# Performance work log

Hardware: AMD Instinct MI355X
Metric: run time of the kernel (lower is better)

Reference implementation:

```python
import jax, jax.numpy as jnp
import numpy as np

C = 256; CM = 8; MAXI = 100; NCLS = 80
KP = (CM + 2) * CM + CM + CM * CM + CM + CM + 1  # 169 dynamic-kernel params

def _ln(x, g, b, eps=1e-5):
    m = x.mean(-1, keepdims=True)
    v = ((x - m) ** 2).mean(-1, keepdims=True)
    return g * (x - m) * jax.lax.rsqrt(v + eps) + b

def _mlp(x, hw, hb, lng, lnb, fw, fb):
    # torchvision MLP: [Linear -> LayerNorm -> SiLU] * n_hidden -> Linear
    for i in range(hw.shape[0]):
        x = jax.nn.silu(_ln(x @ hw[i] + hb[i], lng[i], lnb[i]))
    return x @ fw + fb

def _conv1x1_bn(x, w, s, b):
    # 1x1 conv (no bias) + inference-mode BatchNorm folded into per-channel affine
    y = jnp.einsum('bchw,oc->bohw', x, w)
    return y * s[None, :, None, None] + b[None, :, None, None]

def _grid(h, w):
    # normalized cell-center coordinates, (x, y) order, shape [h, w, 2]
    ys = (jnp.arange(h, dtype=jnp.float32) + 0.5) / h
    xs = (jnp.arange(w, dtype=jnp.float32) + 0.5) / w
    return jnp.stack([jnp.broadcast_to(xs[None, :], (h, w)),
                      jnp.broadcast_to(ys[:, None], (h, w))], axis=-1)

def setup_inputs() -> dict:
    key = jax.random.key(0)
    ks = iter(jax.random.split(key, 40))
    nrm = lambda shape, s=0.02: s * jax.random.normal(next(ks), shape, jnp.float32)
    B = 4
    inp = {
        'x0': jax.random.normal(next(ks), (B, 3, 512, 512), jnp.float32),
        'x1': jax.random.normal(next(ks), (B, 64, 256, 256), jnp.float32),
        'x2': jax.random.normal(next(ks), (B, 128, 128, 128), jnp.float32),
        'x3': jax.random.normal(next(ks), (B, 256, 64, 64), jnp.float32),
        'x4': jax.random.normal(next(ks), (B, 512, 32, 32), jnp.float32),
        'x5': jax.random.normal(next(ks), (B, 1024, 16, 16), jnp.float32),
        'lat3_w': nrm((C, 256)), 'lat3_s': jnp.ones((C,)), 'lat3_b': jnp.zeros((C,)),
        'lat4_w': nrm((C, 512)), 'lat4_s': jnp.ones((C,)), 'lat4_b': jnp.zeros((C,)),
        'lat5_w': nrm((C, 1024)), 'lat5_s': jnp.ones((C,)), 'lat5_b': jnp.zeros((C,)),
        'mlat_w': nrm((C, 256)), 'mlat_s': jnp.ones((C,)), 'mlat_b': jnp.zeros((C,)),
        'mhead_w': nrm((CM, C, 3, 3)), 'mhead_s': jnp.ones((CM,)), 'mhead_b': jnp.zeros((CM,)),
        'loc_hw': nrm((4, C, C)), 'loc_hb': jnp.zeros((4, C)), 'loc_lng': jnp.ones((4, C)), 'loc_lnb': jnp.zeros((4, C)),
        'loc_fw': nrm((C, 1)), 'loc_fb': -5.0 * jnp.ones((1,)),
        'cls_hw': nrm((4, C, C)), 'cls_hb': jnp.zeros((4, C)), 'cls_lng': jnp.ones((4, C)), 'cls_lnb': jnp.zeros((4, C)),
        'cls_fw': nrm((C, NCLS)), 'cls_fb': jnp.zeros((NCLS,)),
        'ker_hw': nrm((4, C, C)), 'ker_hb': jnp.zeros((4, C)), 'ker_lng': jnp.ones((4, C)), 'ker_lnb': jnp.zeros((4, C)),
        'ker_fw': nrm((C, KP)), 'ker_fb': jnp.zeros((KP,)),
    }
    return inp

def reference(x0, x1, x2, x3, x4, x5,
              lat3_w, lat3_s, lat3_b, lat4_w, lat4_s, lat4_b, lat5_w, lat5_s, lat5_b,
              mlat_w, mlat_s, mlat_b, mhead_w, mhead_s, mhead_b,
              loc_hw, loc_hb, loc_lng, loc_lnb, loc_fw, loc_fb,
              cls_hw, cls_hb, cls_lng, cls_lnb, cls_fw, cls_fb,
              ker_hw, ker_hb, ker_lng, ker_lnb, ker_fw, ker_fb):
    B, _, H, W = x0.shape
    lvls = [(x3, lat3_w, lat3_s, lat3_b), (x4, lat4_w, lat4_s, lat4_b), (x5, lat5_w, lat5_s, lat5_b)]
    feats = [_conv1x1_bn(x, w, s, b) for (x, w, s, b) in lvls]
    flat = jnp.concatenate([f.reshape(B, C, -1).transpose(0, 2, 1) for f in feats], axis=1)  # [B, L, C]
    loc_logits = _mlp(flat, loc_hw, loc_hb, loc_lng, loc_lnb, loc_fw, loc_fb)[..., 0]       # [B, L]
    top_vals, top_idx = jax.lax.top_k(loc_logits, MAXI)
    scores = jax.nn.sigmoid(top_vals)
    num_instances = (scores > 0.5).sum(axis=1)
    gfeat = jnp.take_along_axis(flat, top_idx[:, :, None], axis=1)  # [B, I, C]
    # mask branch
    mf = _conv1x1_bn(x3, mlat_w, mlat_s, mlat_b)
    mf = jax.lax.conv_general_dilated(mf, mhead_w, (1, 1), 'SAME', dimension_numbers=('NCHW', 'OIHW', 'NCHW'))
    mf = jax.nn.silu(mf * mhead_s[None, :, None, None] + mhead_b[None, :, None, None])  # [B, CM, h3, w3]
    h3, w3 = x3.shape[2], x3.shape[3]
    offs_flat = jnp.concatenate([_grid(x.shape[2], x.shape[3]).reshape(-1, 2) for x in (x3, x4, x5)], axis=0)
    offs = offs_flat[top_idx]                                # [B, I, 2]
    grid = _grid(h3, w3).transpose(2, 0, 1)                  # [2, h3, w3]
    grid = grid[None, None] - offs[:, :, :, None, None]      # [B, I, 2, h, w]
    mfi = jnp.broadcast_to(mf[:, None], (B, MAXI, CM, h3, w3))
    feats_i = jnp.concatenate([mfi, grid], axis=2)           # [B, I, CM+2, h, w]
    dyn = _mlp(gfeat, ker_hw, ker_hb, ker_lng, ker_lnb, ker_fw, ker_fb)  # [B, I, KP]
    c = CM
    o = (c + 2) * c
    w1 = dyn[..., :o].reshape(B, MAXI, c + 2, c)
    b1 = dyn[..., o:o + c].reshape(B, MAXI, c, 1, 1); o += c
    w2 = dyn[..., o:o + c * c].reshape(B, MAXI, c, c); o += c * c
    b2 = dyn[..., o:o + c].reshape(B, MAXI, c, 1, 1); o += c
    w3 = dyn[..., o:o + c].reshape(B, MAXI, c, 1); o += c
    b3 = dyn[..., o:].reshape(B, MAXI, 1, 1, 1)
    m = jax.nn.silu(jnp.einsum('bichw,bicd->bidhw', feats_i, w1) + b1)
    m = jax.nn.silu(jnp.einsum('bichw,bicd->bidhw', m, w2) + b2)
    m = jnp.einsum('bichw,bicd->bidhw', m, w3) + b3
    masks = jax.nn.sigmoid(m[:, :, 0])                       # [B, I, h3, w3]
    classes = jnp.argmax(_mlp(gfeat, cls_hw, cls_hb, cls_lng, cls_lnb, cls_fw, cls_fb), axis=-1)
    masks = jax.image.resize(masks, (B, MAXI, H, W), method='bilinear', antialias=False)
    return (num_instances, scores, classes, masks)
```

## Files before the change

### kernel.cpp

```cpp
#include <hip/hip_runtime.h>
#include <hip/hip_bf16.h>
#include <math.h>

#define DEVI __device__ __forceinline__

constexpr int LTOT  = 5376;
constexpr int NINST = 100;
constexpr int NCLS  = 80;
constexpr int KPAR  = 169;

DEVI float waveAllSum(float v) {
#pragma unroll
  for (int s = 32; s > 0; s >>= 1) v += __shfl_xor(v, s, 64);
  return v;
}
DEVI float siluf(float x) { return x / (1.0f + expf(-x)); }
DEVI float sigmf(float x) { return 1.0f / (1.0f + expf(-x)); }
DEVI float rdlane(float v, int lane) {
  return __int_as_float(__builtin_amdgcn_readlane(__float_as_int(v), lane));
}

__global__ __launch_bounds__(256) void wtrans(
    const float* __restrict__ w3, const float* __restrict__ w4,
    const float* __restrict__ w5, const float* __restrict__ wm,
    float* __restrict__ wt3, float* __restrict__ wt4,
    float* __restrict__ wt5, float* __restrict__ wtm)
{
  __shared__ float t[64][65];
  const int bid = blockIdx.x;
  const float* src; float* dst; int K, rel;
  if (bid < 16)       { src = w3; dst = wt3; K = 256;  rel = bid; }
  else if (bid < 48)  { src = w4; dst = wt4; K = 512;  rel = bid - 16; }
  else if (bid < 112) { src = w5; dst = wt5; K = 1024; rel = bid - 48; }
  else                { src = wm; dst = wtm; K = 256;  rel = bid - 112; }
  const int ctiles = K >> 6;
  const int ot = rel / ctiles, ct = rel % ctiles;
  const int o0 = ot * 64, c0 = ct * 64;
  const int tid = threadIdx.x;
#pragma unroll
  for (int s = 0; s < 16; ++s) {
    const int e = tid + 256*s;
    const int r = e >> 6, c = e & 63;
    t[r][c] = src[(long)(o0 + r)*K + c0 + c];
  }
  __syncthreads();
#pragma unroll
  for (int s = 0; s < 16; ++s) {
    const int e = tid + 256*s;
    const int q = e >> 6, p = e & 63;
    dst[(long)(c0 + q)*256 + o0 + p] = t[p][q];
  }
}

__global__ __launch_bounds__(256) void lateral_main(
    const float* __restrict__ x3, const float* __restrict__ x4, const float* __restrict__ x5,
    const float* __restrict__ wt3, const float* __restrict__ s3, const float* __restrict__ b3,
    const float* __restrict__ wt4, const float* __restrict__ s4, const float* __restrict__ b4,
    const float* __restrict__ wt5, const float* __restrict__ s5, const float* __restrict__ b5,
    const float* __restrict__ wtm, const float* __restrict__ sm, const float* __restrict__ bm,
    float* __restrict__ flat, float* __restrict__ mlatb)
{
  __shared__ float xs[32][36];
  __shared__ float ws[32][256];
  const int tid = threadIdx.x;
  const int rg = tid >> 6, cg = tid & 63;
  const int bid = blockIdx.x;
  const float *x, *wt, *sc, *bi;
  int K, P, b, p0, baseL = 0; bool tomlat = false;
  if (bid < 512)       { x=x3; wt=wt3; sc=s3; bi=b3; K=256;  P=4096; b=bid>>7;  p0=(bid&127)*32; }
  else if (bid < 1024) { const int rel=bid-512;  x=x3; wt=wtm; sc=sm; bi=bm; K=256;  P=4096; b=rel>>7; p0=(rel&127)*32; tomlat=true; }
  else if (bid < 1152) { const int rel=bid-1024; x=x4; wt=wt4; sc=s4; bi=b4; K=512;  P=1024; b=rel>>5; p0=(rel&31)*32; baseL=4096; }
  else                 { const int rel=bid-1152; x=x5; wt=wt5; sc=s5; bi=b5; K=1024; P=256;  b=rel>>3; p0=(rel&7)*32;  baseL=5120; }
  const float* xb = x + (long)b * K * P;
  float acc[8][4] = {};
  const int nkb = K >> 5;
  for (int kb = 0; kb < nkb; ++kb) {
    __syncthreads();
#pragma unroll
    for (int s = 0; s < 4; ++s) {
      const int e = tid + 256*s;
      const int kk = e >> 5, px = e & 31;
      xs[kk][px] = xb[(long)(kb*32 + kk)*P + p0 + px];
    }
    {
      const float4* w4p = reinterpret_cast<const float4*>(wt + (kb << 13));
#pragma unroll
      for (int q = 0; q < 8; ++q) {
        const int c = tid + (q << 8);
        *reinterpret_cast<float4*>(&ws[c >> 6][4*(c & 63)]) = w4p[c];
      }
    }
    __syncthreads();
#pragma unroll
    for (int kk = 0; kk < 32; ++kk) {
      const float4 a0 = *reinterpret_cast<const float4*>(&xs[kk][8*rg]);
      const float4 a1 = *reinterpret_cast<const float4*>(&xs[kk][8*rg+4]);
      const float ar[8] = {a0.x,a0.y,a0.z,a0.w,a1.x,a1.y,a1.z,a1.w};
      const float4 wv = *reinterpret_cast<const float4*>(&ws[kk][4*cg]);
#pragma unroll
      for (int i = 0; i < 8; ++i) {
        acc[i][0] += ar[i]*wv.x; acc[i][1] += ar[i]*wv.y;
        acc[i][2] += ar[i]*wv.z; acc[i][3] += ar[i]*wv.w;
      }
    }
  }
  const float4 sA = *reinterpret_cast<const float4*>(&sc[4*cg]);
  const float4 bA = *reinterpret_cast<const float4*>(&bi[4*cg]);
  if (!tomlat) {
#pragma unroll
    for (int i = 0; i < 8; ++i) {
      const float4 ov = { acc[i][0]*sA.x+bA.x, acc[i][1]*sA.y+bA.y,
                          acc[i][2]*sA.z+bA.z, acc[i][3]*sA.w+bA.w };
      *reinterpret_cast<float4*>(&flat[((long)b*LTOT + baseL + p0 + 8*rg + i)*256 + 4*cg]) = ov;
    }
  } else {
#pragma unroll
    for (int j = 0; j < 4; ++j) {
      const float sj = (&sA.x)[j], bj = (&bA.x)[j];
      const float4 o0 = { acc[0][j]*sj+bj, acc[1][j]*sj+bj, acc[2][j]*sj+bj, acc[3][j]*sj+bj };
      const float4 o1 = { acc[4][j]*sj+bj, acc[5][j]*sj+bj, acc[6][j]*sj+bj, acc[7][j]*sj+bj };
      float* mb = &mlatb[((long)b*256 + 4*cg + j)*4096 + p0 + 8*rg];
      *reinterpret_cast<float4*>(mb) = o0;
      *reinterpret_cast<float4*>(mb + 4) = o1;
    }
  }
}

__global__ __launch_bounds__(256, 4) void loc4(
    const float* __restrict__ in, const float* __restrict__ hw,
    const float* __restrict__ hb, const float* __restrict__ lng, const float* __restrict__ lnb,
    const float* __restrict__ fw, const float* __restrict__ fb, float* __restrict__ logits)
{
  const int tid = threadIdx.x;
  const int rg = tid >> 6, cg = tid & 63;
  const long r0 = (long)blockIdx.x * 32 + rg * 8;
  float xv[8][4];
#pragma unroll
  for (int i = 0; i < 8; ++i) {
    const float4 v = *reinterpret_cast<const float4*>(&in[(r0 + i)*256 + 4*cg]);
    xv[i][0]=v.x; xv[i][1]=v.y; xv[i][2]=v.z; xv[i][3]=v.w;
  }
  for (int L = 0; L < 4; ++L) {
    const float* w = hw + L*65536 + 4*cg;
    float acc[8][4] = {};
    for (int kb = 0; kb < 256; kb += 8) {
      float4 wv[8];
#pragma unroll
      for (int u = 0; u < 8; ++u)
        wv[u] = *reinterpret_cast<const float4*>(&w[(kb + u) << 8]);
#pragma unroll
      for (int u = 0; u < 8; ++u) {
        const int lanek = (kb >> 2) + (u >> 2);
#pragma unroll
        for (int i = 0; i < 8; ++i) {
          const float a = rdlane(xv[i][u & 3], lanek);
          acc[i][0] += a*wv[u].x; acc[i][1] += a*wv[u].y;
          acc[i][2] += a*wv[u].z; acc[i][3] += a*wv[u].w;
        }
      }
    }
    const float4 hb4 = *reinterpret_cast<const float4*>(&hb[L*256 + 4*cg]);
    const float4 g4  = *reinterpret_cast<const float4*>(&lng[L*256 + 4*cg]);
    const float4 lb4 = *reinterpret_cast<const float4*>(&lnb[L*256 + 4*cg]);
#pragma unroll
    for (int i = 0; i < 8; ++i) {
      const float y0 = acc[i][0]+hb4.x, y1 = acc[i][1]+hb4.y;
      const float y2 = acc[i][2]+hb4.z, y3 = acc[i][3]+hb4.w;
      const float m = waveAllSum(y0+y1+y2+y3) * (1.0f/256.0f);
      const float d0=y0-m, d1=y1-m, d2=y2-m, d3=y3-m;
      const float var = waveAllSum(d0*d0+d1*d1+d2*d2+d3*d3) * (1.0f/256.0f);
      const float rs = rsqrtf(var + 1e-5f);
      xv[i][0] = siluf(g4.x*d0*rs + lb4.x);
      xv[i][1] = siluf(g4.y*d1*rs + lb4.y);
      xv[i][2] = siluf(g4.z*d2*rs + lb4.z);
      xv[i][3] = siluf(g4.w*d3*rs + lb4.w);
    }
  }
  const float4 fw4 = *reinterpret_cast<const float4*>(&fw[4*cg]);
  const float fbv = fb[0];
#pragma unroll
  for (int i = 0; i < 8; ++i) {
    float d = xv[i][0]*fw4.x + xv[i][1]*fw4.y + xv[i][2]*fw4.z + xv[i][3]*fw4.w;
    d = waveAllSum(d);
    if (cg == 0) logits[r0 + i] = d + fbv;
  }
}

__global__ __launch_bounds__(256) void topk_gather(
    const float* __restrict__ logits, const float* __restrict__ flat,
    int* __restrict__ topi, float* __restrict__ gfeat,
    float* __restrict__ dout)
{
  __shared__ float sv[LTOT];
  __shared__ float rv[4];
  __shared__ int   ri[4];
  __shared__ int   sidx[NINST];
  const int b = blockIdx.x, tid = threadIdx.x;
  for (int l = tid; l < LTOT; l += 256) sv[l] = logits[b*LTOT + l];
  __syncthreads();
  int cnt = 0;
  for (int t = 0; t < NINST; ++t) {
    float bv = -INFINITY; int bidx = 0x7fffffff;
    for (int l = tid; l < LTOT; l += 256) {
      const float v = sv[l];
      if (v > bv) { bv = v; bidx = l; }
    }
#pragma unroll
    for (int s = 32; s > 0; s >>= 1) {
      const float v2 = __shfl_xor(bv, s, 64);
      const int   i2 = __shfl_xor(bidx, s, 64);
      if (v2 > bv || (v2 == bv && i2 < bidx)) { bv = v2; bidx = i2; }
    }
    if ((tid & 63) == 0) { rv[tid >> 6] = bv; ri[tid >> 6] = bidx; }
    __syncthreads();
    if (tid == 0) {
      bv = rv[0]; bidx = ri[0];
#pragma unroll
      for (int q = 1; q < 4; ++q)
        if (rv[q] > bv || (rv[q] == bv && ri[q] < bidx)) { bv = rv[q]; bidx = ri[q]; }
      sidx[t] = bidx; topi[b*NINST + t] = bidx;
      dout[4 + b*NINST + t] = sigmf(bv);
      if (bv > 0.0f) ++cnt;
      sv[bidx] = -INFINITY;
    }
    __syncthreads();
  }
  if (tid == 0) dout[b] = (float)cnt;
  for (int t = 0; t < NINST; ++t) {
    const int ix = sidx[t];
    gfeat[((long)b*NINST + t)*256 + tid] = flat[((long)b*LTOT + ix)*256 + tid];
  }
}

__global__ __launch_bounds__(256) void clsker4(
    const float* __restrict__ gfeat, float* __restrict__ h2,
    const float* __restrict__ chw, const float* __restrict__ chb,
    const float* __restrict__ cg_, const float* __restrict__ cb_,
    const float* __restrict__ khw, const float* __restrict__ khb,
    const float* __restrict__ kg_, const float* __restrict__ kb_)
{
  __shared__ float xs[256][12];
  __shared__ float wsm[16][256];
  const int tid = threadIdx.x;
  const int rg = tid >> 6, cg = tid & 63;
  const bool ker = blockIdx.x >= 50;
  const int r0 = (ker ? (blockIdx.x - 50) : blockIdx.x) * 8;
  const int outr0 = r0 + (ker ? 400 : 0);
  const float* hw = ker ? khw : chw;
  const float* hb = ker ? khb : chb;
  const float* g_ = ker ? kg_ : cg_;
  const float* lb = ker ? kb_ : cb_;
#pragma unroll
  for (int s = 0; s < 2; ++s) {
    const int e = tid + 256*s;
    const int row = e >> 6, q = e & 63;
    const float4 v = *reinterpret_cast<const float4*>(&gfeat[(long)(r0 + row)*256 + 4*q]);
    const int pc = 2*((row >> 1) ^ (q & 3)) + (row & 1);
#pragma unroll
    for (int j = 0; j < 4; ++j) xs[4*q+j][pc] = (&v.x)[j];
  }
  float ov[2][4];
  for (int L = 0; L < 4; ++L) {
    const float* w = hw + L*65536;
    float acc[2][4] = {};
    for (int kb = 0; kb < 16; ++kb) {
      __syncthreads();
      const float4* w4 = reinterpret_cast<const float4*>(w + (kb << 12));
#pragma unroll
      for (int q = 0; q < 4; ++q) {
        const int c = tid + (q << 8);
        *reinterpret_cast<float4*>(&wsm[c>>6][4*(c&63)]) = w4[c];
      }
      __syncthreads();
#pragma unroll
      for (int kk = 0; kk < 16; ++kk) {
        const int k = (kb << 4) + kk;
        const float2 av = *reinterpret_cast<const float2*>(&xs[k][2*(rg ^ ((k >> 2) & 3))]);
        const float4 wv = *reinterpret_cast<const float4*>(&wsm[kk][4*cg]);
        acc[0][0] += av.x*wv.x; acc[0][1] += av.x*wv.y; acc[0][2] += av.x*wv.z; acc[0][3] += av.x*wv.w;
        acc[1][0] += av.y*wv.x; acc[1][1] += av.y*wv.y; acc[1][2] += av.y*wv.z; acc[1][3] += av.y*wv.w;
      }
    }
    const float4 hb4 = *reinterpret_cast<const float4*>(&hb[L*256 + 4*cg]);
    const float4 g4  = *reinterpret_cast<const float4*>(&g_[L*256 + 4*cg]);
    const float4 lb4 = *reinterpret_cast<const float4*>(&lb[L*256 + 4*cg]);
#pragma unroll
    for (int i = 0; i < 2; ++i) {
      const float y0 = acc[i][0]+hb4.x, y1 = acc[i][1]+hb4.y;
      const float y2 = acc[i][2]+hb4.z, y3 = acc[i][3]+hb4.w;
      const float m = waveAllSum(y0+y1+y2+y3) * (1.0f/256.0f);
      const float d0=y0-m, d1=y1-m, d2=y2-m, d3=y3-m;
      const float var = waveAllSum(d0*d0+d1*d1+d2*d2+d3*d3) * (1.0f/256.0f);
      const float rs = rsqrtf(var + 1e-5f);
      ov[i][0] = siluf(g4.x*d0*rs + lb4.x);
      ov[i][1] = siluf(g4.y*d1*rs + lb4.y);
      ov[i][2] = siluf(g4.z*d2*rs + lb4.z);
      ov[i][3] = siluf(g4.w*d3*rs + lb4.w);
    }
    __syncthreads();
    if (L < 3) {
      const int pc = 2*(rg ^ (cg & 3));
#pragma unroll
      for (int j = 0; j < 4; ++j) {
        const float2 t = {ov[0][j], ov[1][j]};
        *reinterpret_cast<float2*>(&xs[4*cg+j][pc]) = t;
      }
    }
  }
#pragma unroll
  for (int i = 0; i < 2; ++i) {
    const float4 o = {ov[i][0], ov[i][1], ov[i][2], ov[i][3]};
    *reinterpret_cast<float4*>(&h2[(long)(outr0 + 2*rg + i)*256 + 4*cg]) = o;
  }
}

__global__ __launch_bounds__(256) void heads(
    const float* __restrict__ h2, const float* __restrict__ cfw, const float* __restrict__ cfb,
    const float* __restrict__ kfw, const float* __restrict__ kfb,
    float* __restrict__ dout, float* __restrict__ dyn)
{
  __shared__ float xr[256];
  __shared__ float lv[NCLS];
  const int bid = blockIdx.x, tid = threadIdx.x;
  xr[tid] = h2[(long)bid*256 + tid];
  __syncthreads();
  if (bid < 400) {
    if (tid < NCLS) {
      float a0=0.f, a1=0.f, a2=0.f, a3=0.f;
      for (int k = 0; k < 256; k += 4) {
        a0 += xr[k+0]*cfw[(k+0)*NCLS + tid];
        a1 += xr[k+1]*cfw[(k+1)*NCLS + tid];
        a2 += xr[k+2]*cfw[(k+2)*NCLS + tid];
        a3 += xr[k+3]*cfw[(k+3)*NCLS + tid];
      }
      lv[tid] = (a0+a1) + (a2+a3) + cfb[tid];
    }
    __syncthreads();
    if (tid == 0) {
      float bv = lv[0]; int bi2 = 0;
      for (int o = 1; o < NCLS; ++o) if (lv[o] > bv) { bv = lv[o]; bi2 = o; }
      dout[404 + bid] = (float)bi2;
    }
  } else {
    if (tid < KPAR) {
      float a0=0.f, a1=0.f, a2=0.f, a3=0.f;
      for (int k = 0; k < 256; k += 4) {
        a0 += xr[k+0]*kfw[(k+0)*KPAR + tid];
        a1 += xr[k+1]*kfw[(k+1)*KPAR + tid];
        a2 += xr[k+2]*kfw[(k+2)*KPAR + tid];
        a3 += xr[k+3]*kfw[(k+3)*KPAR + tid];
      }
      dyn[(long)(bid-400)*KPAR + tid] = (a0+a1) + (a2+a3) + kfb[tid];
    }
  }
}

__global__ __launch_bounds__(256) void conv3(
    const float* __restrict__ mlat, const float* __restrict__ mw,
    float* __restrict__ partial)
{
  const int bid = blockIdx.x;
  const int cc = bid & 7;
  const int tile = (bid >> 3) & 15;
  const int b = bid >> 7;
  const int y0 = (tile >> 2)*16, x0 = (tile & 3)*16;
  const int tid = threadIdx.x;
  const int ly = tid >> 4, lx = tid & 15;
  __shared__ float til[2][18][19];
  __shared__ float wch[8][32][12];
  for (int e = tid; e < 2304; e += 256) {
    const int o = e / 288, rem = e % 288;
    const int c = rem / 9, qq = rem - c*9;
    wch[o][c][qq] = mw[((o*256) + cc*32 + c)*9 + qq];
  }
  int lofs[3], gofs[3], chn[3]; bool vld[3], has[3];
  float* tf = &til[0][0][0];
#pragma unroll
  for (int s = 0; s < 3; ++s) {
    const int e = tid + 256*s;
    has[s] = (e < 648);
    lofs[s] = 0; gofs[s] = 0; chn[s] = 0; vld[s] = false;
    if (has[s]) {
      const int ch = (e >= 324) ? 1 : 0;
      const int pos = e - ch*324;
      const int iy = pos / 18, ix = pos - iy*18;
      const int gy = y0 - 1 + iy, gx = x0 - 1 + ix;
      vld[s] = (gy >= 0 && gy < 64 && gx >= 0 && gx < 64);
      lofs[s] = ch*342 + iy*19 + ix;
      gofs[s] = gy*64 + gx;
      chn[s] = ch;
    }
  }
  const float* xbase = mlat + ((long)b*256 + cc*32)*4096;
  float acc[8] = {};
  for (int r = 0; r < 16; ++r) {
    __syncthreads();
#pragma unroll
    for (int s = 0; s < 3; ++s)
      if (has[s]) tf[lofs[s]] = vld[s] ? xbase[(long)(2*r + chn[s])*4096 + gofs[s]] : 0.f;
    __syncthreads();
#pragma unroll
    for (int ch = 0; ch < 2; ++ch) {
      const int c = 2*r + ch;
      float t[9];
#pragma unroll
      for (int dy = 0; dy < 3; ++dy)
#pragma unroll
        for (int dx = 0; dx < 3; ++dx) t[dy*3+dx] = til[ch][ly+dy][lx+dx];
#pragma unroll
      for (int o = 0; o < 8; ++o) {
        const float4 wa = *reinterpret_cast<const float4*>(&wch[o][c][0]);
        const float4 wb = *reinterpret_cast<const float4*>(&wch[o][c][4]);
        const float w8 = wch[o][c][8];
        acc[o] += t[0]*wa.x + t[1]*wa.y + t[2]*wa.z + t[3]*wa.w
                + t[4]*wb.x + t[5]*wb.y + t[6]*wb.z + t[7]*wb.w + t[8]*w8;
      }
    }
  }
  const long pbase = (((long)b*8 + cc)*8)*4096 + (y0+ly)*64 + (x0+lx);
#pragma unroll
  for (int o = 0; o < 8; ++o) partial[pbase + (long)o*4096] = acc[o];
}

__global__ __launch_bounds__(256) void mhead_fin(
    const float* __restrict__ partial, const float* __restrict__ s,
    const float* __restrict__ bi, float* __restrict__ mhead)
{
  const int idx = blockIdx.x*256 + threadIdx.x;
  const int p = idx & 4095;
  const int o = (idx >> 12) & 7;
  const int b = idx >> 15;
  float v = 0.f;
#pragma unroll
  for (int cc = 0; cc < 8; ++cc) v += partial[(((long)b*8 + cc)*8 + o)*4096 + p];
  v = v*s[o] + bi[o];
  mhead[idx] = siluf(v);
}

__global__ __launch_bounds__(256) void mask_fused(
    const float* __restrict__ dyn, const int* __restrict__ topi,
    const float* __restrict__ mhead, float* __restrict__ dout)
{
  __shared__ float msrc[18][64];
  __shared__ float dd[KPAR];
  __shared__ float so[2];
  const int bid = blockIdx.x;
  const int inst = bid >> 2, q = bid & 3;
  const int tid = threadIdx.x;
  if (tid < KPAR) dd[tid] = dyn[(long)inst*KPAR + tid];
  if (tid == 0) {
    const int l = topi[inst];
    float ox, oy;
    if (l < 4096)      { ox = ((l & 63) + 0.5f)*(1.f/64.f); oy = ((l >> 6) + 0.5f)*(1.f/64.f); }
    else if (l < 5120) { const int t = l - 4096; ox = ((t & 31) + 0.5f)*(1.f/32.f); oy = ((t >> 5) + 0.5f)*(1.f/32.f); }
    else               { const int t = l - 5120; ox = ((t & 15) + 0.5f)*(1.f/16.f); oy = ((t >> 4) + 0.5f)*(1.f/16.f); }
    so[0] = ox; so[1] = oy;
  }
  __syncthreads();
  const float ox = so[0], oy = so[1];
  const int b = inst / NINST;
  const float* mh = mhead + (long)b*8*4096;
  const int r0s = 16*q - 1;
  for (int e = tid; e < 1152; e += 256) {
    const int r = e >> 6, x = e & 63;
    int sy = r0s + r; sy = sy < 0 ? 0 : (sy > 63 ? 63 : sy);
    const int p = sy*64 + x;
    float f[10];
#pragma unroll
    for (int c = 0; c < 8; ++c) f[c] = mh[c*4096 + p];
    f[8] = (x + 0.5f)*(1.f/64.f) - ox;
    f[9] = (sy + 0.5f)*(1.f/64.f) - oy;
    float m1[8];
#pragma unroll
    for (int d = 0; d < 8; ++d) {
      float t = dd[80 + d];
#pragma unroll
      for (int c = 0; c < 10; ++c) t += f[c]*dd[c*8 + d];
      m1[d] = siluf(t);
    }
    float m2[8];
#pragma unroll
    for (int d = 0; d < 8; ++d) {
      float t = dd[152 + d];
#pragma unroll
      for (int c = 0; c < 8; ++c) t += m1[c]*dd[88 + c*8 + d];
      m2[d] = siluf(t);
    }
    float o = dd[168];
#pragma unroll
    for (int c = 0; c < 8; ++c) o += m2[c]*dd[160 + c];
    msrc[r][x] = sigmf(o);
  }
  __syncthreads();
  const int j4 = tid & 127;
  const int half = tid >> 7;
  const int ix0 = (j4 & 1) ? (j4 >> 1) : (j4 >> 1) - 1;
  const int xlo = ix0 < 0 ? 0 : ix0;
  const int xhi = (ix0 + 1 > 63) ? 63 : ix0 + 1;
  float fx[4];
#pragma unroll
  for (int m = 0; m < 4; ++m) {
    const int x = 4*j4 + m;
    const float tx = (x + 0.5f)*0.125f - 0.5f;
    fx[m] = tx - (float)ix0;
  }
  float* dbase = dout + 804 + ((long)inst << 18);
  for (int it = 0; it < 64; ++it) {
    const int yy = 2*it + half;
    const int y = 128*q + yy;
    const float ty = (y + 0.5f)*0.125f - 0.5f;
    const float fyf = floorf(ty);
    const int iy0 = (int)fyf;
    const float fy = ty - fyf;
    const int r0 = iy0 - r0s;
    const float L0 = msrc[r0][xlo],   R0 = msrc[r0][xhi];
    const float L1 = msrc[r0+1][xlo], R1 = msrc[r0+1][xhi];
    const float L = L0 + (L1 - L0)*fy;
    const float R = R0 + (R1 - R0)*fy;
    const float4 ovv = { L + (R - L)*fx[0], L + (R - L)*fx[1],
                         L + (R - L)*fx[2], L + (R - L)*fx[3] };
    *reinterpret_cast<float4*>(&dbase[((long)y << 9) + (j4 << 2)]) = ovv;
  }
}

extern "C" void kernel_launch(void* const* d_in, const int* in_sizes, int n_in,
                              void* d_out, int out_size, void* d_ws, size_t ws_size,
                              hipStream_t stream)
{
  (void)in_sizes; (void)n_in; (void)out_size; (void)ws_size;
  const float* x3      = (const float*)d_in[3];
  const float* x4      = (const float*)d_in[4];
  const float* x5      = (const float*)d_in[5];
  const float* lat3_w  = (const float*)d_in[6];
  const float* lat3_s  = (const float*)d_in[7];
  const float* lat3_b  = (const float*)d_in[8];
  const float* lat4_w  = (const float*)d_in[9];
  const float* lat4_s  = (const float*)d_in[10];
  const float* lat4_b  = (const float*)d_in[11];
  const float* lat5_w  = (const float*)d_in[12];
  const float* lat5_s  = (const float*)d_in[13];
  const float* lat5_b  = (const float*)d_in[14];
  const float* mlat_w  = (const float*)d_in[15];
  const float* mlat_s  = (const float*)d_in[16];
  const float* mlat_b  = (const float*)d_in[17];
  const float* mhead_w = (const float*)d_in[18];
  const float* mhead_s = (const float*)d_in[19];
  const float* mhead_b = (const float*)d_in[20];
  const float* loc_hw  = (const float*)d_in[21];
  const float* loc_hb  = (const float*)d_in[22];
  const float* loc_lng = (const float*)d_in[23];
  const float* loc_lnb = (const float*)d_in[24];
  const float* loc_fw  = (const float*)d_in[25];
  const float* loc_fb  = (const float*)d_in[26];
  const float* cls_hw  = (const float*)d_in[27];
  const float* cls_hb  = (const float*)d_in[28];
  const float* cls_lng = (const float*)d_in[29];
  const float* cls_lnb = (const float*)d_in[30];
  const float* cls_fw  = (const float*)d_in[31];
  const float* cls_fb  = (const float*)d_in[32];
  const float* ker_hw  = (const float*)d_in[33];
  const float* ker_hb  = (const float*)d_in[34];
  const float* ker_lng = (const float*)d_in[35];
  const float* ker_lnb = (const float*)d_in[36];
  const float* ker_fw  = (const float*)d_in[37];
  const float* ker_fb  = (const float*)d_in[38];

  float* ws      = (float*)d_ws;
  float* flat    = ws;
  float* mlatb   = ws + 5505024;
  float* partial = ws + 9699328;
  float* mheadb  = ws + 10747904;
  float* h2      = ws + 10878976;
  float* logits  = ws + 11083776;
  int*   topi    = (int*)(ws + 11105280);
  float* gfeat   = ws + 11105680;
  float* dynb    = ws + 11208080;
  float* wt3     = ws + 11275680;
  float* wt4     = ws + 11341216;
  float* wt5     = ws + 11472288;
  float* wtm     = ws + 11734432;
  float* dout    = (float*)d_out;

  wtrans<<<128, 256, 0, stream>>>(lat3_w, lat4_w, lat5_w, mlat_w, wt3, wt4, wt5, wtm);
  lateral_main<<<1184, 256, 0, stream>>>(x3, x4, x5,
      wt3, lat3_s, lat3_b, wt4, lat4_s, lat4_b, wt5, lat5_s, lat5_b,
      wtm, mlat_s, mlat_b, flat, mlatb);
  conv3<<<512, 256, 0, stream>>>(mlatb, mhead_w, partial);
  mhead_fin<<<512, 256, 0, stream>>>(partial, mhead_s, mhead_b, mheadb);
  loc4<<<672, 256, 0, stream>>>(flat, loc_hw, loc_hb, loc_lng, loc_lnb,
                                loc_fw, loc_fb, logits);
  topk_gather<<<4, 256, 0, stream>>>(logits, flat, topi, gfeat, dout);
  clsker4<<<100, 256, 0, stream>>>(gfeat, h2,
      cls_hw, cls_hb, cls_lng, cls_lnb, ker_hw, ker_hb, ker_lng, ker_lnb);
  heads<<<800, 256, 0, stream>>>(h2, cls_fw, cls_fb, ker_fw, ker_fb, dout, dynb);
  mask_fused<<<1600, 256, 0, stream>>>(dynb, topi, mheadb, dout);
}
```

Baseline: 810.7 us.

## Stage loc MLP activations in LDS instead of cross-lane readlane broadcasts

The loc-head MLP kernel now keeps each wave's row activations in shared memory and reads them back as float4 broadcasts, instead of holding them in registers and broadcasting with readlane. It also switches to 7 rows per wave, relaxes launch bounds to 3 blocks, and launches 768 blocks so the rows still divide exactly. This is meant to remove the scalar readlane traffic and its dependence stalls in the inner FMA loop. In exchange it adds LDS traffic, a 28 KB shared footprint, and fewer rows sharing each weight load.

```diff
diff --git a/kernel.cpp b/kernel.cpp
--- a/kernel.cpp
+++ b/kernel.cpp
@@ -16,9 +16,6 @@
 }
 DEVI float siluf(float x) { return x / (1.0f + expf(-x)); }
 DEVI float sigmf(float x) { return 1.0f / (1.0f + expf(-x)); }
-DEVI float rdlane(float v, int lane) {
-  return __int_as_float(__builtin_amdgcn_readlane(__float_as_int(v), lane));
-}
 
 __global__ __launch_bounds__(256) void wtrans(
     const float* __restrict__ w3, const float* __restrict__ w4,
@@ -126,36 +123,53 @@
   }
 }
 
-__global__ __launch_bounds__(256, 4) void loc4(
+__global__ __launch_bounds__(256, 3) void loc4(
     const float* __restrict__ in, const float* __restrict__ hw,
     const float* __restrict__ hb, const float* __restrict__ lng, const float* __restrict__ lnb,
     const float* __restrict__ fw, const float* __restrict__ fb, float* __restrict__ logits)
 {
+  __shared__ float xls[4][7][256];
   const int tid = threadIdx.x;
   const int rg = tid >> 6, cg = tid & 63;
-  const long r0 = (long)blockIdx.x * 32 + rg * 8;
-  float xv[8][4];
-#pragma unroll
-  for (int i = 0; i < 8; ++i) {
-    const float4 v = *reinterpret_cast<const float4*>(&in[(r0 + i)*256 + 4*cg]);
-    xv[i][0]=v.x; xv[i][1]=v.y; xv[i][2]=v.z; xv[i][3]=v.w;
-  }
+  const int r0 = blockIdx.x * 28 + rg * 7;
+  float* xw = &xls[rg][0][0];
+#pragma unroll
+  for (int i = 0; i < 7; ++i) {
+    const float4 v = *reinterpret_cast<const float4*>(&in[(long)(r0 + i)*256 + 4*cg]);
+    *reinterpret_cast<float4*>(&xw[i*256 + 4*cg]) = v;
+  }
+  const float4 fw4 = *reinterpret_cast<const float4*>(&fw[4*cg]);
+  const float fbv = fb[0];
   for (int L = 0; L < 4; ++L) {
     const float* w = hw + L*65536 + 4*cg;
-    float acc[8][4] = {};
+    float acc[7][4] = {};
     for (int kb = 0; kb < 256; kb += 8) {
       float4 wv[8];
 #pragma unroll
       for (int u = 0; u < 8; ++u)
         wv[u] = *reinterpret_cast<const float4*>(&w[(kb + u) << 8]);
-#pragma unroll
-      for (int u = 0; u < 8; ++u) {
-        const int lanek = (kb >> 2) + (u >> 2);
-#pragma unroll
-        for (int i = 0; i < 8; ++i) {
-          const float a = rdlane(xv[i][u & 3], lanek);
-          acc[i][0] += a*wv[u].x; acc[i][1] += a*wv[u].y;
-          acc[i][2] += a*wv[u].z; acc[i][3] += a*wv[u].w;
+      float4 av[7], bv[7];
+#pragma unroll
+      for (int r = 0; r < 7; ++r) {
+        av[r] = *reinterpret_cast<const float4*>(&xw[r*256 + kb]);
+        bv[r] = *reinterpret_cast<const float4*>(&xw[r*256 + kb + 4]);
+      }
+#pragma unroll
+      for (int u = 0; u < 4; ++u) {
+#pragma unroll
+        for (int r = 0; r < 7; ++r) {
+          const float a = (&av[r].x)[u];
+          acc[r][0] += a*wv[u].x; acc[r][1] += a*wv[u].y;
+          acc[r][2] += a*wv[u].z; acc[r][3] += a*wv[u].w;
+        }
+      }
+#pragma unroll
+      for (int u = 0; u < 4; ++u) {
+#pragma unroll
+        for (int r = 0; r < 7; ++r) {
+          const float a = (&bv[r].x)[u];
+          acc[r][0] += a*wv[u+4].x; acc[r][1] += a*wv[u+4].y;
+          acc[r][2] += a*wv[u+4].z; acc[r][3] += a*wv[u+4].w;
         }
       }
     }
@@ -163,26 +177,26 @@
     const float4 g4  = *reinterpret_cast<const float4*>(&lng[L*256 + 4*cg]);
     const float4 lb4 = *reinterpret_cast<const float4*>(&lnb[L*256 + 4*cg]);
 #pragma unroll
-    for (int i = 0; i < 8; ++i) {
-      const float y0 = acc[i][0]+hb4.x, y1 = acc[i][1]+hb4.y;
-      const float y2 = acc[i][2]+hb4.z, y3 = acc[i][3]+hb4.w;
+    for (int r = 0; r < 7; ++r) {
+      const float y0 = acc[r][0]+hb4.x, y1 = acc[r][1]+hb4.y;
+      const float y2 = acc[r][2]+hb4.z, y3 = acc[r][3]+hb4.w;
       const float m = waveAllSum(y0+y1+y2+y3) * (1.0f/256.0f);
       const float d0=y0-m, d1=y1-m, d2=y2-m, d3=y3-m;
       const float var = waveAllSum(d0*d0+d1*d1+d2*d2+d3*d3) * (1.0f/256.0f);
       const float rs = rsqrtf(var + 1e-5f);
-      xv[i][0] = siluf(g4.x*d0*rs + lb4.x);
-      xv[i][1] = siluf(g4.y*d1*rs + lb4.y);
-      xv[i][2] = siluf(g4.z*d2*rs + lb4.z);
-      xv[i][3] = siluf(g4.w*d3*rs + lb4.w);
-    }
-  }
-  const float4 fw4 = *reinterpret_cast<const float4*>(&fw[4*cg]);
-  const float fbv = fb[0];
-#pragma unroll
-  for (int i = 0; i < 8; ++i) {
-    float d = xv[i][0]*fw4.x + xv[i][1]*fw4.y + xv[i][2]*fw4.z + xv[i][3]*fw4.w;
-    d = waveAllSum(d);
-    if (cg == 0) logits[r0 + i] = d + fbv;
+      const float o0 = siluf(g4.x*d0*rs + lb4.x);
+      const float o1 = siluf(g4.y*d1*rs + lb4.y);
+      const float o2 = siluf(g4.z*d2*rs + lb4.z);
+      const float o3 = siluf(g4.w*d3*rs + lb4.w);
+      if (L < 3) {
+        const float4 ov = {o0, o1, o2, o3};
+        *reinterpret_cast<float4*>(&xw[r*256 + 4*cg]) = ov;
+      } else {
+        float d = o0*fw4.x + o1*fw4.y + o2*fw4.z + o3*fw4.w;
+        d = waveAllSum(d);
+        if (cg == 0) logits[r0 + r] = d + fbv;
+      }
+    }
   }
 }
 
@@ -587,7 +601,7 @@
       wtm, mlat_s, mlat_b, flat, mlatb);
   conv3<<<512, 256, 0, stream>>>(mlatb, mhead_w, partial);
   mhead_fin<<<512, 256, 0, stream>>>(partial, mhead_s, mhead_b, mheadb);
-  loc4<<<672, 256, 0, stream>>>(flat, loc_hw, loc_hb, loc_lng, loc_lnb,
+  loc4<<<768, 256, 0, stream>>>(flat, loc_hw, loc_hb, loc_lng, loc_lnb,
                                 loc_fw, loc_fb, logits);
   topk_gather<<<4, 256, 0, stream>>>(logits, flat, topi, gfeat, dout);
   clsker4<<<100, 256, 0, stream>>>(gfeat, h2,
```

Result: no change. 809.3 us (-0.2%).
